# Kernel tuning notes

Measured on AMD Instinct MI355X. Metric: run time of the kernel, lower is better.

## Reference

```python
import jax, jax.numpy as jnp
import numpy as np

N_NODES = 100000


def gcn_conv(x, W, b, src, dst, num_nodes):
    # PyG GCNConv: add self-loops, symmetric normalization, x @ W, scatter-add, + b
    xw = x @ W  # [N, out]
    loop = jnp.arange(num_nodes, dtype=src.dtype)
    s = jnp.concatenate([src, loop])  # message source j
    d = jnp.concatenate([dst, loop])  # aggregation target i
    deg = jax.ops.segment_sum(jnp.ones_like(d, dtype=xw.dtype), d, num_segments=num_nodes)
    dis = jnp.where(deg > 0, jax.lax.rsqrt(deg), 0.0)  # D^{-1/2}
    norm = dis[s] * dis[d]  # [E+N]
    msg = norm[:, None] * xw[s]  # gather + scale
    out = jax.ops.segment_sum(msg, d, num_segments=num_nodes)  # scatter-add
    return out + b


def setup_inputs() -> dict:
    key = jax.random.key(0)
    k1, k2, k3, k4 = jax.random.split(key, 4)
    F, H, E = 64, 64, 1250000
    x = jax.random.normal(k1, (N_NODES, F), dtype=jnp.float32)
    edge_index = jax.random.randint(k2, (2, E), 0, N_NODES, dtype=jnp.int64)
    W1 = jax.random.normal(k3, (F, H), dtype=jnp.float32) * (1.0 / np.sqrt(F))
    b1 = jnp.zeros((H,), dtype=jnp.float32)
    W2 = jax.random.normal(k4, (H, F), dtype=jnp.float32) * (1.0 / np.sqrt(H))
    b2 = jnp.zeros((F,), dtype=jnp.float32)
    return {"x": x, "edge_index": edge_index, "W1": W1, "b1": b1, "W2": W2, "b2": b2}


def reference(x, edge_index, W1, b1, W2, b2):
    src, dst = edge_index[0], edge_index[1]
    h = gcn_conv(x, W1, b1, src, dst, N_NODES)
    h = jax.nn.relu(h)
    out = gcn_conv(h, W2, b2, src, dst, N_NODES)
    return out
```

## Files before the change

kernel.cpp:

```cpp
#include <hip/hip_runtime.h>

#define NN    100000
#define F     64
#define NBUCK 391
#define CAPB  4096
#define TILE  4096
#define G1A   1600
#define G1TOT 3125

#define O_CURSOR 0
#define O_ROWPTR 512
#define O_DEG    100864
#define O_DIS    201216
#define O_PACKED 301568
#define O_SRT    1903104
#define O_AH     3504768
#define O_BH     6704768

__device__ __forceinline__ unsigned bf_rne(float x) {
    unsigned u = __float_as_uint(x);
    return (u + 0x7FFFu + ((u >> 16) & 1u)) >> 16;
}
__device__ __forceinline__ unsigned pack2(float lo, float hi) {
    return bf_rne(lo) | (bf_rne(hi) << 16);
}
__device__ __forceinline__ float lo_f(unsigned u) { return __uint_as_float(u << 16); }
__device__ __forceinline__ float hi_f(unsigned u) { return __uint_as_float(u & 0xFFFF0000u); }

struct BpSmem {
    int hist[NBUCK], lofs[NBUCK], gbase[NBUCK], lcur[NBUCK];
    int wsum[8];
    unsigned stage[TILE];
    unsigned short sbuck[TILE];
};
union KSmem {
    BpSmem bp;
    float wl[64 * 64];
};
struct NsSmem {
    int h[256], lcur[256], wsum[4];
    int stage[CAPB];
};
union K2Smem {
    NsSmem ns;
    float wl[64 * 64];
};

__device__ __forceinline__ void binpack_body(const int* __restrict__ src,
                                             const int* __restrict__ dst, int E,
                                             int* __restrict__ cursor,
                                             unsigned* __restrict__ packed,
                                             int bid, BpSmem& sm) {
    int t  = threadIdx.x;
    int t0 = bid * TILE;
    int n  = min(TILE, E - t0);

    if (t < NBUCK) sm.hist[t] = 0;
    __syncthreads();
    for (int i = t; i < n; i += 512) atomicAdd(&sm.hist[dst[t0 + i] >> 8], 1);
    __syncthreads();
    int lane = t & 63, w = t >> 6;
    int v = (t < NBUCK) ? sm.hist[t] : 0;
    int s = v;
#pragma unroll
    for (int off = 1; off < 64; off <<= 1) {
        int u = __shfl_up(s, off, 64);
        if (lane >= off) s += u;
    }
    if (lane == 63) sm.wsum[w] = s;
    __syncthreads();
    if (t == 0) {
        int run = 0;
#pragma unroll
        for (int i = 0; i < 8; ++i) { int c = sm.wsum[i]; sm.wsum[i] = run; run += c; }
    }
    __syncthreads();
    if (t < NBUCK) {
        int ex = s - v + sm.wsum[w];
        sm.lofs[t] = ex;
        sm.lcur[t] = ex;
        sm.gbase[t] = t * CAPB + (v ? atomicAdd(&cursor[t], v) : 0);
    }
    __syncthreads();
    for (int i = t; i < n; i += 512) {
        int d = dst[t0 + i];
        int b = d >> 8;
        int p = atomicAdd(&sm.lcur[b], 1);
        sm.stage[p] = ((unsigned)src[t0 + i] << 8) | (unsigned)(d & 255);
        sm.sbuck[p] = (unsigned short)b;
    }
    __syncthreads();
    for (int i = t; i < n; i += 512) {
        int b = sm.sbuck[i];
        packed[sm.gbase[b] + (i - sm.lofs[b])] = sm.stage[i];
    }
}

__device__ __forceinline__ void gemm_body(const float* __restrict__ X,
                                          const float* __restrict__ W,
                                          unsigned* __restrict__ Ah, int bid,
                                          float* wl) {
    int t = threadIdx.x;
    for (int i = t; i < 64 * 64; i += 512) wl[i] = W[i];
    __syncthreads();
    int lane = t & 63;
    int w    = t >> 6;
    float Wreg[64];
#pragma unroll
    for (int k = 0; k < 64; ++k) Wreg[k] = wl[k * 64 + lane];

    int row0 = bid * 32 + w * 4;
    const float* xp = X + (size_t)row0 * F;
    float xa = xp[lane];
    float xb = xp[64 + lane];
    float xc = xp[128 + lane];
    float xd = xp[192 + lane];
    float a0 = 0.f, a1 = 0.f, a2 = 0.f, a3 = 0.f;
#pragma unroll
    for (int k = 0; k < 64; ++k) {
        float wv = Wreg[k];
        a0 = fmaf(__uint_as_float(__builtin_amdgcn_readlane(__float_as_uint(xa), k)), wv, a0);
        a1 = fmaf(__uint_as_float(__builtin_amdgcn_readlane(__float_as_uint(xb), k)), wv, a1);
        a2 = fmaf(__uint_as_float(__builtin_amdgcn_readlane(__float_as_uint(xc), k)), wv, a2);
        a3 = fmaf(__uint_as_float(__builtin_amdgcn_readlane(__float_as_uint(xd), k)), wv, a3);
    }
    float p0 = __shfl_xor(a0, 1, 64);
    float p1 = __shfl_xor(a1, 1, 64);
    float p2 = __shfl_xor(a2, 1, 64);
    float p3 = __shfl_xor(a3, 1, 64);
    if (!(lane & 1)) {
        int c = lane >> 1;
        Ah[(size_t)(row0 + 0) * 32 + c] = pack2(a0, p0);
        Ah[(size_t)(row0 + 1) * 32 + c] = pack2(a1, p1);
        Ah[(size_t)(row0 + 2) * 32 + c] = pack2(a2, p2);
        Ah[(size_t)(row0 + 3) * 32 + c] = pack2(a3, p3);
    }
}

__device__ __forceinline__ void node_sort_body(const unsigned* __restrict__ packed,
                                               const int* __restrict__ cursor,
                                               int* __restrict__ row_ptr,
                                               int* __restrict__ deg,
                                               float* __restrict__ dis,
                                               int* __restrict__ srt,
                                               int b, NsSmem& sm) {
    int t = threadIdx.x;
    int nbase = b << 8;
    int nloc = min(256, NN - nbase);
    int beg = b * CAPB;
    int n = cursor[b];

    if (t < 256) sm.h[t] = 0;
    __syncthreads();
    for (int i = t; i < n; i += 512)
        atomicAdd(&sm.h[packed[beg + i] & 255u], 1);
    __syncthreads();
    int lane = t & 63, w = t >> 6;
    int v = 0, s = 0;
    if (t < 256) { v = sm.h[t]; s = v; }
#pragma unroll
    for (int off = 1; off < 64; off <<= 1) {
        int u = __shfl_up(s, off, 64);
        if (lane >= off) s += u;
    }
    if (t < 256 && lane == 63) sm.wsum[w] = s;
    __syncthreads();
    if (t == 0) {
        int run = 0;
#pragma unroll
        for (int i = 0; i < 4; ++i) { int c = sm.wsum[i]; sm.wsum[i] = run; run += c; }
    }
    __syncthreads();
    if (t < 256) {
        int e0 = s - v + sm.wsum[w];
        sm.lcur[t] = e0;
        if (t < nloc) {
            row_ptr[nbase + t] = beg + e0;
            deg[nbase + t]     = v;
            dis[nbase + t]     = rsqrtf((float)v + 1.0f);
        }
    }
    __syncthreads();
    for (int i = t; i < n; i += 512) {
        unsigned p = packed[beg + i];
        int pos = atomicAdd(&sm.lcur[p & 255u], 1);
        sm.stage[pos] = (int)(p >> 8);
    }
    __syncthreads();
    for (int i = t; i < n; i += 512) srt[beg + i] = sm.stage[i];
}

__global__ __launch_bounds__(512) void pre_gemm1(const int* __restrict__ src,
                                                 const int* __restrict__ dst, int E,
                                                 int nbp, int* __restrict__ cursor,
                                                 unsigned* __restrict__ packed,
                                                 const float* __restrict__ X,
                                                 const float* __restrict__ W1,
                                                 unsigned* __restrict__ Ah) {
    __shared__ KSmem sm;
    if ((int)blockIdx.x < nbp)
        binpack_body(src, dst, E, cursor, packed, blockIdx.x, sm.bp);
    else
        gemm_body(X, W1, Ah, (int)blockIdx.x - nbp, sm.wl);
}

__global__ __launch_bounds__(512) void sort_gemm1(const unsigned* __restrict__ packed,
                                                  const int* __restrict__ cursor,
                                                  int* __restrict__ row_ptr,
                                                  int* __restrict__ deg,
                                                  float* __restrict__ dis,
                                                  int* __restrict__ srt,
                                                  const float* __restrict__ X,
                                                  const float* __restrict__ W1,
                                                  unsigned* __restrict__ Ah) {
    __shared__ K2Smem sm;
    if ((int)blockIdx.x < NBUCK)
        node_sort_body(packed, cursor, row_ptr, deg, dis, srt, blockIdx.x, sm.ns);
    else
        gemm_body(X, W1, Ah, G1A + (int)blockIdx.x - NBUCK, sm.wl);
}

__global__ __launch_bounds__(256) void agg1_gemm2(const uint4* __restrict__ Ah4,
                                                  const int* __restrict__ row_ptr,
                                                  const int* __restrict__ deg,
                                                  const int* __restrict__ srt,
                                                  const float* __restrict__ dis,
                                                  const float* __restrict__ b1,
                                                  const float* __restrict__ W2,
                                                  unsigned* __restrict__ Bh) {
    __shared__ float wl[64 * 64];
    int t = threadIdx.x;
    for (int i = t; i < 1024; i += 256)
        ((float4*)wl)[i] = ((const float4*)W2)[i];
    __syncthreads();

    int sub  = t & 7;
    int grp  = (t >> 3) & 1;
    int node = blockIdx.x * 16 + (t >> 4);
    int beg = row_ptr[node];
    int end = beg + deg[node];
    float di = dis[node];

    float a0, a1, a2, a3, a4, a5, a6, a7;
    uint4 su = Ah4[(size_t)node * 8 + sub];
    if (grp == 0) {
        a0 = di * lo_f(su.x); a1 = di * hi_f(su.x);
        a2 = di * lo_f(su.y); a3 = di * hi_f(su.y);
        a4 = di * lo_f(su.z); a5 = di * hi_f(su.z);
        a6 = di * lo_f(su.w); a7 = di * hi_f(su.w);
    } else {
        a0 = a1 = a2 = a3 = a4 = a5 = a6 = a7 = 0.f;
    }

    int j = beg + grp;
    for (; j + 6 < end; j += 8) {
        int s0 = srt[j], s1 = srt[j + 2], s2 = srt[j + 4], s3 = srt[j + 6];
        float d0 = dis[s0], d1 = dis[s1], d2 = dis[s2], d3 = dis[s3];
        uint4 g0 = Ah4[(size_t)s0 * 8 + sub];
        uint4 g1 = Ah4[(size_t)s1 * 8 + sub];
        uint4 g2 = Ah4[(size_t)s2 * 8 + sub];
        uint4 g3 = Ah4[(size_t)s3 * 8 + sub];
        a0 = fmaf(d0, lo_f(g0.x), fmaf(d1, lo_f(g1.x), fmaf(d2, lo_f(g2.x), fmaf(d3, lo_f(g3.x), a0))));
        a1 = fmaf(d0, hi_f(g0.x), fmaf(d1, hi_f(g1.x), fmaf(d2, hi_f(g2.x), fmaf(d3, hi_f(g3.x), a1))));
        a2 = fmaf(d0, lo_f(g0.y), fmaf(d1, lo_f(g1.y), fmaf(d2, lo_f(g2.y), fmaf(d3, lo_f(g3.y), a2))));
        a3 = fmaf(d0, hi_f(g0.y), fmaf(d1, hi_f(g1.y), fmaf(d2, hi_f(g2.y), fmaf(d3, hi_f(g3.y), a3))));
        a4 = fmaf(d0, lo_f(g0.z), fmaf(d1, lo_f(g1.z), fmaf(d2, lo_f(g2.z), fmaf(d3, lo_f(g3.z), a4))));
        a5 = fmaf(d0, hi_f(g0.z), fmaf(d1, hi_f(g1.z), fmaf(d2, hi_f(g2.z), fmaf(d3, hi_f(g3.z), a5))));
        a6 = fmaf(d0, lo_f(g0.w), fmaf(d1, lo_f(g1.w), fmaf(d2, lo_f(g2.w), fmaf(d3, lo_f(g3.w), a6))));
        a7 = fmaf(d0, hi_f(g0.w), fmaf(d1, hi_f(g1.w), fmaf(d2, hi_f(g2.w), fmaf(d3, hi_f(g3.w), a7))));
    }
    for (; j + 2 < end; j += 4) {
        int s0 = srt[j], s1 = srt[j + 2];
        float d0 = dis[s0], d1 = dis[s1];
        uint4 g0 = Ah4[(size_t)s0 * 8 + sub];
        uint4 g1 = Ah4[(size_t)s1 * 8 + sub];
        a0 = fmaf(d0, lo_f(g0.x), fmaf(d1, lo_f(g1.x), a0));
        a1 = fmaf(d0, hi_f(g0.x), fmaf(d1, hi_f(g1.x), a1));
        a2 = fmaf(d0, lo_f(g0.y), fmaf(d1, lo_f(g1.y), a2));
        a3 = fmaf(d0, hi_f(g0.y), fmaf(d1, hi_f(g1.y), a3));
        a4 = fmaf(d0, lo_f(g0.z), fmaf(d1, lo_f(g1.z), a4));
        a5 = fmaf(d0, hi_f(g0.z), fmaf(d1, hi_f(g1.z), a5));
        a6 = fmaf(d0, lo_f(g0.w), fmaf(d1, lo_f(g1.w), a6));
        a7 = fmaf(d0, hi_f(g0.w), fmaf(d1, hi_f(g1.w), a7));
    }
    for (; j < end; j += 2) {
        int s0 = srt[j];
        float d0 = dis[s0];
        uint4 g0 = Ah4[(size_t)s0 * 8 + sub];
        a0 = fmaf(d0, lo_f(g0.x), a0);
        a1 = fmaf(d0, hi_f(g0.x), a1);
        a2 = fmaf(d0, lo_f(g0.y), a2);
        a3 = fmaf(d0, hi_f(g0.y), a3);
        a4 = fmaf(d0, lo_f(g0.z), a4);
        a5 = fmaf(d0, hi_f(g0.z), a5);
        a6 = fmaf(d0, lo_f(g0.w), a6);
        a7 = fmaf(d0, hi_f(g0.w), a7);
    }
    a0 += __shfl_xor(a0, 8, 64); a1 += __shfl_xor(a1, 8, 64);
    a2 += __shfl_xor(a2, 8, 64); a3 += __shfl_xor(a3, 8, 64);
    a4 += __shfl_xor(a4, 8, 64); a5 += __shfl_xor(a5, 8, 64);
    a6 += __shfl_xor(a6, 8, 64); a7 += __shfl_xor(a7, 8, 64);

    float4 bb0 = ((const float4*)b1)[2 * sub];
    float4 bb1 = ((const float4*)b1)[2 * sub + 1];
    float o0 = fmaxf(fmaf(di, a0, bb0.x), 0.f);
    float o1 = fmaxf(fmaf(di, a1, bb0.y), 0.f);
    float o2 = fmaxf(fmaf(di, a2, bb0.z), 0.f);
    float o3 = fmaxf(fmaf(di, a3, bb0.w), 0.f);
    float o4 = fmaxf(fmaf(di, a4, bb1.x), 0.f);
    float o5 = fmaxf(fmaf(di, a5, bb1.y), 0.f);
    float o6 = fmaxf(fmaf(di, a6, bb1.z), 0.f);
    float o7 = fmaxf(fmaf(di, a7, bb1.w), 0.f);
    unsigned pk0 = pack2(o0, o1);
    unsigned pk1 = pack2(o2, o3);
    unsigned pk2 = pack2(o4, o5);
    unsigned pk3 = pack2(o6, o7);

    int lane = t & 63;
    float c0 = 0.f, c1 = 0.f, c2 = 0.f, c3 = 0.f;
#pragma unroll
    for (int l8 = 0; l8 < 8; ++l8) {
#define STEP(PK, P)                                                        \
        {                                                                  \
            int k0 = l8 * 8 + 2 * (P);                                     \
            float w0 = wl[k0 * 64 + lane];                                 \
            float w1 = wl[k0 * 64 + 64 + lane];                            \
            unsigned u0 = __builtin_amdgcn_readlane(PK, l8);               \
            unsigned u1 = __builtin_amdgcn_readlane(PK, 16 + l8);          \
            unsigned u2 = __builtin_amdgcn_readlane(PK, 32 + l8);          \
            unsigned u3 = __builtin_amdgcn_readlane(PK, 48 + l8);          \
            c0 = fmaf(lo_f(u0), w0, c0); c0 = fmaf(hi_f(u0), w1, c0);      \
            c1 = fmaf(lo_f(u1), w0, c1); c1 = fmaf(hi_f(u1), w1, c1);      \
            c2 = fmaf(lo_f(u2), w0, c2); c2 = fmaf(hi_f(u2), w1, c2);      \
            c3 = fmaf(lo_f(u3), w0, c3); c3 = fmaf(hi_f(u3), w1, c3);      \
        }
        STEP(pk0, 0)
        STEP(pk1, 1)
        STEP(pk2, 2)
        STEP(pk3, 3)
#undef STEP
    }
    float dA = __shfl(di, 0, 64);
    float dB = __shfl(di, 16, 64);
    float dC = __shfl(di, 32, 64);
    float dD = __shfl(di, 48, 64);
    c0 *= dA; c1 *= dB; c2 *= dC; c3 *= dD;
    float q0 = __shfl_xor(c0, 1, 64);
    float q1 = __shfl_xor(c1, 1, 64);
    float q2 = __shfl_xor(c2, 1, 64);
    float q3 = __shfl_xor(c3, 1, 64);
    if (!(lane & 1)) {
        int c = lane >> 1;
        int n0 = blockIdx.x * 16 + (t >> 6) * 4;
        Bh[(size_t)(n0 + 0) * 32 + c] = pack2(c0, q0);
        Bh[(size_t)(n0 + 1) * 32 + c] = pack2(c1, q1);
        Bh[(size_t)(n0 + 2) * 32 + c] = pack2(c2, q2);
        Bh[(size_t)(n0 + 3) * 32 + c] = pack2(c3, q3);
    }
}

__global__ __launch_bounds__(256) void agg_out(const uint4* __restrict__ Bs4,
                                               const int* __restrict__ row_ptr,
                                               const int* __restrict__ deg,
                                               const int* __restrict__ srt,
                                               const float* __restrict__ dis,
                                               const float* __restrict__ bias,
                                               float* __restrict__ outp) {
    int t = threadIdx.x;
    int sub  = t & 7;
    int grp  = (t >> 3) & 1;
    int node = blockIdx.x * 16 + (t >> 4);
    int beg = row_ptr[node];
    int end = beg + deg[node];
    float di = dis[node];

    float a0, a1, a2, a3, a4, a5, a6, a7;
    uint4 su = Bs4[(size_t)node * 8 + sub];
    if (grp == 0) {
        a0 = lo_f(su.x); a1 = hi_f(su.x);
        a2 = lo_f(su.y); a3 = hi_f(su.y);
        a4 = lo_f(su.z); a5 = hi_f(su.z);
        a6 = lo_f(su.w); a7 = hi_f(su.w);
    } else {
        a0 = a1 = a2 = a3 = a4 = a5 = a6 = a7 = 0.f;
    }

    int j = beg + grp;
    for (; j + 6 < end; j += 8) {
        int s0 = srt[j], s1 = srt[j + 2], s2 = srt[j + 4], s3 = srt[j + 6];
        uint4 g0 = Bs4[(size_t)s0 * 8 + sub];
        uint4 g1 = Bs4[(size_t)s1 * 8 + sub];
        uint4 g2 = Bs4[(size_t)s2 * 8 + sub];
        uint4 g3 = Bs4[(size_t)s3 * 8 + sub];
        a0 += (lo_f(g0.x) + lo_f(g1.x)) + (lo_f(g2.x) + lo_f(g3.x));
        a1 += (hi_f(g0.x) + hi_f(g1.x)) + (hi_f(g2.x) + hi_f(g3.x));
        a2 += (lo_f(g0.y) + lo_f(g1.y)) + (lo_f(g2.y) + lo_f(g3.y));
        a3 += (hi_f(g0.y) + hi_f(g1.y)) + (hi_f(g2.y) + hi_f(g3.y));
        a4 += (lo_f(g0.z) + lo_f(g1.z)) + (lo_f(g2.z) + lo_f(g3.z));
        a5 += (hi_f(g0.z) + hi_f(g1.z)) + (hi_f(g2.z) + hi_f(g3.z));
        a6 += (lo_f(g0.w) + lo_f(g1.w)) + (lo_f(g2.w) + lo_f(g3.w));
        a7 += (hi_f(g0.w) + hi_f(g1.w)) + (hi_f(g2.w) + hi_f(g3.w));
    }
    for (; j + 2 < end; j += 4) {
        int s0 = srt[j], s1 = srt[j + 2];
        uint4 g0 = Bs4[(size_t)s0 * 8 + sub];
        uint4 g1 = Bs4[(size_t)s1 * 8 + sub];
        a0 += lo_f(g0.x) + lo_f(g1.x);
        a1 += hi_f(g0.x) + hi_f(g1.x);
        a2 += lo_f(g0.y) + lo_f(g1.y);
        a3 += hi_f(g0.y) + hi_f(g1.y);
        a4 += lo_f(g0.z) + lo_f(g1.z);
        a5 += hi_f(g0.z) + hi_f(g1.z);
        a6 += lo_f(g0.w) + lo_f(g1.w);
        a7 += hi_f(g0.w) + hi_f(g1.w);
    }
    for (; j < end; j += 2) {
        int s0 = srt[j];
        uint4 g0 = Bs4[(size_t)s0 * 8 + sub];
        a0 += lo_f(g0.x); a1 += hi_f(g0.x);
        a2 += lo_f(g0.y); a3 += hi_f(g0.y);
        a4 += lo_f(g0.z); a5 += hi_f(g0.z);
        a6 += lo_f(g0.w); a7 += hi_f(g0.w);
    }
    a0 += __shfl_xor(a0, 8, 64); a1 += __shfl_xor(a1, 8, 64);
    a2 += __shfl_xor(a2, 8, 64); a3 += __shfl_xor(a3, 8, 64);
    a4 += __shfl_xor(a4, 8, 64); a5 += __shfl_xor(a5, 8, 64);
    a6 += __shfl_xor(a6, 8, 64); a7 += __shfl_xor(a7, 8, 64);

    float4 bb0 = ((const float4*)bias)[2 * sub];
    float4 bb1 = ((const float4*)bias)[2 * sub + 1];
    float4 o;
    if (grp == 0) {
        o.x = fmaf(di, a0, bb0.x);
        o.y = fmaf(di, a1, bb0.y);
        o.z = fmaf(di, a2, bb0.z);
        o.w = fmaf(di, a3, bb0.w);
        ((float4*)outp)[(size_t)node * 16 + 2 * sub] = o;
    } else {
        o.x = fmaf(di, a4, bb1.x);
        o.y = fmaf(di, a5, bb1.y);
        o.z = fmaf(di, a6, bb1.z);
        o.w = fmaf(di, a7, bb1.w);
        ((float4*)outp)[(size_t)node * 16 + 2 * sub + 1] = o;
    }
}

extern "C" void kernel_launch(void* const* d_in, const int* in_sizes, int n_in,
                              void* d_out, int out_size, void* d_ws, size_t ws_size,
                              hipStream_t stream) {
    const float* x  = (const float*)d_in[0];
    const int*   ei = (const int*)d_in[1];
    const float* W1 = (const float*)d_in[2];
    const float* b1 = (const float*)d_in[3];
    const float* W2 = (const float*)d_in[4];
    const float* b2 = (const float*)d_in[5];
    float* out = (float*)d_out;
    int E = in_sizes[1] / 2;
    const int* src = ei;
    const int* dst = ei + E;

    int*      ws_i    = (int*)d_ws;
    int*      cursor  = ws_i + O_CURSOR;
    int*      row_ptr = ws_i + O_ROWPTR;
    int*      deg     = ws_i + O_DEG;
    float*    dis     = (float*)(ws_i + O_DIS);
    unsigned* packed  = (unsigned*)(ws_i + O_PACKED);
    int*      srt     = ws_i + O_SRT;
    unsigned* Ah      = (unsigned*)(ws_i + O_AH);
    unsigned* Bh      = (unsigned*)(ws_i + O_BH);

    int nbp = (E + TILE - 1) / TILE;

    hipMemsetAsync(cursor, 0, NBUCK * sizeof(int), stream);
    pre_gemm1<<<nbp + G1A, 512, 0, stream>>>(src, dst, E, nbp, cursor, packed,
                                             x, W1, Ah);
    sort_gemm1<<<NBUCK + (G1TOT - G1A), 512, 0, stream>>>(packed, cursor, row_ptr,
                                                          deg, dis, srt, x, W1, Ah);
    agg1_gemm2<<<NN / 16, 256, 0, stream>>>((const uint4*)Ah, row_ptr, deg, srt,
                                            dis, b1, W2, Bh);
    agg_out<<<NN / 16, 256, 0, stream>>>((const uint4*)Bh, row_ptr, deg, srt,
                                         dis, b2, out);
}
```

Before: 193.1 us.

## Use MFMA bf16 for fused second GEMM and register-cache edges in sorts

The per-node 64x64 GEMM in the agg1_gemm2 kernel moves from scalar FMAs with readlane broadcasts to MFMA 16x16x32 bf16 instructions. Hidden activations are staged through a swizzled LDS buffer, and W2 is split into high and low bf16 parts so the matrix product keeps near-fp32 weight precision. The binpack and node-sort phases also keep their loaded edges in registers between the histogram and scatter passes instead of reading global memory twice. In exchange the kernel does more LDS staging, adds an extra barrier, and assumes each tile holds at most 4096 edges.

```diff
diff --git a/kernel.cpp b/kernel.cpp
--- a/kernel.cpp
+++ b/kernel.cpp
@@ -16,6 +16,9 @@
 #define O_SRT    1903104
 #define O_AH     3504768
 #define O_BH     6704768
+
+typedef __attribute__((ext_vector_type(8))) short bf16x8;
+typedef __attribute__((ext_vector_type(4))) float f32x4;
 
 __device__ __forceinline__ unsigned bf_rne(float x) {
     unsigned u = __float_as_uint(x);
@@ -45,6 +48,11 @@
     NsSmem ns;
     float wl[64 * 64];
 };
+struct K3Smem {
+    unsigned w2f[16][64][4];
+    unsigned hbuf[16 * 32];
+    float dis_s[16];
+};
 
 __device__ __forceinline__ void binpack_body(const int* __restrict__ src,
                                              const int* __restrict__ dst, int E,
@@ -57,7 +65,16 @@
 
     if (t < NBUCK) sm.hist[t] = 0;
     __syncthreads();
-    for (int i = t; i < n; i += 512) atomicAdd(&sm.hist[dst[t0 + i] >> 8], 1);
+    int d_r[8], s_r[8];
+#pragma unroll
+    for (int it = 0; it < 8; ++it) {
+        int i = t + it * 512;
+        if (i < n) {
+            d_r[it] = dst[t0 + i];
+            s_r[it] = src[t0 + i];
+            atomicAdd(&sm.hist[d_r[it] >> 8], 1);
+        }
+    }
     __syncthreads();
     int lane = t & 63, w = t >> 6;
     int v = (t < NBUCK) ? sm.hist[t] : 0;
@@ -82,12 +99,16 @@
         sm.gbase[t] = t * CAPB + (v ? atomicAdd(&cursor[t], v) : 0);
     }
     __syncthreads();
-    for (int i = t; i < n; i += 512) {
-        int d = dst[t0 + i];
-        int b = d >> 8;
-        int p = atomicAdd(&sm.lcur[b], 1);
-        sm.stage[p] = ((unsigned)src[t0 + i] << 8) | (unsigned)(d & 255);
-        sm.sbuck[p] = (unsigned short)b;
+#pragma unroll
+    for (int it = 0; it < 8; ++it) {
+        int i = t + it * 512;
+        if (i < n) {
+            int d = d_r[it];
+            int b = d >> 8;
+            int p = atomicAdd(&sm.lcur[b], 1);
+            sm.stage[p] = ((unsigned)s_r[it] << 8) | (unsigned)(d & 255);
+            sm.sbuck[p] = (unsigned short)b;
+        }
     }
     __syncthreads();
     for (int i = t; i < n; i += 512) {
@@ -152,8 +173,15 @@
 
     if (t < 256) sm.h[t] = 0;
     __syncthreads();
-    for (int i = t; i < n; i += 512)
-        atomicAdd(&sm.h[packed[beg + i] & 255u], 1);
+    unsigned p_r[8];
+#pragma unroll
+    for (int it = 0; it < 8; ++it) {
+        int i = t + it * 512;
+        if (i < n) {
+            p_r[it] = packed[beg + i];
+            atomicAdd(&sm.h[p_r[it] & 255u], 1);
+        }
+    }
     __syncthreads();
     int lane = t & 63, w = t >> 6;
     int v = 0, s = 0;
@@ -181,10 +209,14 @@
         }
     }
     __syncthreads();
-    for (int i = t; i < n; i += 512) {
-        unsigned p = packed[beg + i];
-        int pos = atomicAdd(&sm.lcur[p & 255u], 1);
-        sm.stage[pos] = (int)(p >> 8);
+#pragma unroll
+    for (int it = 0; it < 8; ++it) {
+        int i = t + it * 512;
+        if (i < n) {
+            unsigned p = p_r[it];
+            int pos = atomicAdd(&sm.lcur[p & 255u], 1);
+            sm.stage[pos] = (int)(p >> 8);
+        }
     }
     __syncthreads();
     for (int i = t; i < n; i += 512) srt[beg + i] = sm.stage[i];
@@ -228,11 +260,25 @@
                                                   const float* __restrict__ b1,
                                                   const float* __restrict__ W2,
                                                   unsigned* __restrict__ Bh) {
-    __shared__ float wl[64 * 64];
+    __shared__ K3Smem sm;
     int t = threadIdx.x;
-    for (int i = t; i < 1024; i += 256)
-        ((float4*)wl)[i] = ((const float4*)W2)[i];
-    __syncthreads();
+    for (int idx = t; idx < 4096; idx += 256) {
+        int slot = idx >> 8;
+        int ks   = (slot >> 1) & 1;
+        int p    = slot & 1;
+        int ct   = slot >> 2;
+        int l    = (idx >> 2) & 63;
+        int j    = idx & 3;
+        int k    = 32 * ks + 8 * (l >> 4) + 2 * j;
+        int col  = 16 * ct + (l & 15);
+        float v0 = W2[k * 64 + col];
+        float v1 = W2[(k + 1) * 64 + col];
+        if (p) {
+            v0 -= __uint_as_float(bf_rne(v0) << 16);
+            v1 -= __uint_as_float(bf_rne(v1) << 16);
+        }
+        sm.w2f[slot][l][j] = pack2(v0, v1);
+    }
 
     int sub  = t & 7;
     int grp  = (t >> 3) & 1;
@@ -311,51 +357,45 @@
     float o5 = fmaxf(fmaf(di, a5, bb1.y), 0.f);
     float o6 = fmaxf(fmaf(di, a6, bb1.z), 0.f);
     float o7 = fmaxf(fmaf(di, a7, bb1.w), 0.f);
-    unsigned pk0 = pack2(o0, o1);
-    unsigned pk1 = pack2(o2, o3);
-    unsigned pk2 = pack2(o4, o5);
-    unsigned pk3 = pack2(o6, o7);
-
-    int lane = t & 63;
-    float c0 = 0.f, c1 = 0.f, c2 = 0.f, c3 = 0.f;
-#pragma unroll
-    for (int l8 = 0; l8 < 8; ++l8) {
-#define STEP(PK, P)                                                        \
-        {                                                                  \
-            int k0 = l8 * 8 + 2 * (P);                                     \
-            float w0 = wl[k0 * 64 + lane];                                 \
-            float w1 = wl[k0 * 64 + 64 + lane];                            \
-            unsigned u0 = __builtin_amdgcn_readlane(PK, l8);               \
-            unsigned u1 = __builtin_amdgcn_readlane(PK, 16 + l8);          \
-            unsigned u2 = __builtin_amdgcn_readlane(PK, 32 + l8);          \
-            unsigned u3 = __builtin_amdgcn_readlane(PK, 48 + l8);          \
-            c0 = fmaf(lo_f(u0), w0, c0); c0 = fmaf(hi_f(u0), w1, c0);      \
-            c1 = fmaf(lo_f(u1), w0, c1); c1 = fmaf(hi_f(u1), w1, c1);      \
-            c2 = fmaf(lo_f(u2), w0, c2); c2 = fmaf(hi_f(u2), w1, c2);      \
-            c3 = fmaf(lo_f(u3), w0, c3); c3 = fmaf(hi_f(u3), w1, c3);      \
-        }
-        STEP(pk0, 0)
-        STEP(pk1, 1)
-        STEP(pk2, 2)
-        STEP(pk3, 3)
-#undef STEP
-    }
-    float dA = __shfl(di, 0, 64);
-    float dB = __shfl(di, 16, 64);
-    float dC = __shfl(di, 32, 64);
-    float dD = __shfl(di, 48, 64);
-    c0 *= dA; c1 *= dB; c2 *= dC; c3 *= dD;
-    float q0 = __shfl_xor(c0, 1, 64);
-    float q1 = __shfl_xor(c1, 1, 64);
-    float q2 = __shfl_xor(c2, 1, 64);
-    float q3 = __shfl_xor(c3, 1, 64);
-    if (!(lane & 1)) {
-        int c = lane >> 1;
-        int n0 = blockIdx.x * 16 + (t >> 6) * 4;
-        Bh[(size_t)(n0 + 0) * 32 + c] = pack2(c0, q0);
-        Bh[(size_t)(n0 + 1) * 32 + c] = pack2(c1, q1);
-        Bh[(size_t)(n0 + 2) * 32 + c] = pack2(c2, q2);
-        Bh[(size_t)(n0 + 3) * 32 + c] = pack2(c3, q3);
+
+    int node15 = t >> 4;
+    if (!(t & 8)) {
+        int unit = sub ^ (node15 & 7);
+        uint4 hv;
+        hv.x = pack2(o0, o1);
+        hv.y = pack2(o2, o3);
+        hv.z = pack2(o4, o5);
+        hv.w = pack2(o6, o7);
+        *(uint4*)&sm.hbuf[node15 * 32 + unit * 4] = hv;
+        if (sub == 0) sm.dis_s[node15] = di;
+    }
+    __syncthreads();
+
+    int lane = t & 63, ct = t >> 6;
+    int row = lane & 15, g = lane >> 4;
+    f32x4 acc = {0.f, 0.f, 0.f, 0.f};
+#pragma unroll
+    for (int ks = 0; ks < 2; ++ks) {
+        int unit = (4 * ks + g) ^ (row & 7);
+        uint4 araw = *(const uint4*)&sm.hbuf[row * 32 + unit * 4];
+        uint4 bhr  = *(const uint4*)&sm.w2f[ct * 4 + ks * 2 + 0][lane][0];
+        uint4 blr  = *(const uint4*)&sm.w2f[ct * 4 + ks * 2 + 1][lane][0];
+        bf16x8 A  = __builtin_bit_cast(bf16x8, araw);
+        bf16x8 Bh_ = __builtin_bit_cast(bf16x8, bhr);
+        bf16x8 Bl_ = __builtin_bit_cast(bf16x8, blr);
+        acc = __builtin_amdgcn_mfma_f32_16x16x32_bf16(A, Bh_, acc, 0, 0, 0);
+        acc = __builtin_amdgcn_mfma_f32_16x16x32_bf16(A, Bl_, acc, 0, 0, 0);
+    }
+    int nbase16 = blockIdx.x * 16;
+#pragma unroll
+    for (int r = 0; r < 4; ++r) {
+        int nd = 4 * g + r;
+        float val = acc[r] * sm.dis_s[nd];
+        float q = __shfl_xor(val, 1, 64);
+        if (!(lane & 1)) {
+            int colp = 8 * ct + ((lane & 15) >> 1);
+            Bh[(size_t)(nbase16 + nd) * 32 + colp] = pack2(val, q);
+        }
     }
 }
 
```

New measurement: 201.2 us. +4.2%, slower.
